# Kernel tuning notes

Hardware: AMD Instinct MI355X
Metric: run time of the kernel (lower is better)

## Reference

```python
import jax, jax.numpy as jnp
import numpy as np

ATOM_FDIM = 133
BOND_FDIM = 147
HIDDEN = 300
DEPTH = 3
N_ATOMS = 100000
N_BONDS = 200000
MAX_NB = 6
N_MOLS = 4000


def setup_inputs() -> dict:
    key = jax.random.key(0)
    ks = jax.random.split(key, 10)
    f_atoms = jax.random.normal(ks[0], (N_ATOMS, ATOM_FDIM), dtype=jnp.float32)
    f_bonds = jax.random.normal(ks[1], (N_BONDS, BOND_FDIM), dtype=jnp.float32)
    a2b = jax.random.randint(ks[2], (N_ATOMS, MAX_NB), 0, N_BONDS)
    b2a = jax.random.randint(ks[3], (N_BONDS,), 0, N_ATOMS)
    b2revb = jax.random.randint(ks[4], (N_BONDS,), 0, N_BONDS)
    atom2mol = jnp.sort(jax.random.randint(ks[5], (N_ATOMS,), 0, N_MOLS))
    s = 1.0 / np.sqrt(HIDDEN)
    W_i = jax.random.uniform(ks[6], (BOND_FDIM, HIDDEN), jnp.float32, -s, s)
    W_h = jax.random.uniform(ks[7], (HIDDEN, HIDDEN), jnp.float32, -s, s)
    W_o_w = jax.random.uniform(ks[8], (ATOM_FDIM + HIDDEN, HIDDEN), jnp.float32, -s, s)
    W_o_b = jax.random.uniform(ks[9], (HIDDEN,), jnp.float32, -s, s)
    return {"f_atoms": f_atoms, "f_bonds": f_bonds, "a2b": a2b, "b2a": b2a,
            "b2revb": b2revb, "atom2mol": atom2mol, "W_i": W_i, "W_h": W_h,
            "W_o_w": W_o_w, "W_o_b": W_o_b}


def reference(f_atoms, f_bonds, a2b, b2a, b2revb, atom2mol, W_i, W_h, W_o_w, W_o_b):
    # input = W_i(f_bonds); message = act(input)
    inp = f_bonds @ W_i                      # [n_bonds, hidden]
    message = jax.nn.relu(inp)
    for _ in range(DEPTH - 1):
        # gather neighbor bond messages per atom and sum: [n_atoms, max_nb, h] -> [n_atoms, h]
        a_message = message[a2b].sum(axis=1)
        rev_message = message[b2revb]        # [n_bonds, hidden]
        message = a_message[b2a] - rev_message
        message = jax.nn.relu(inp + message @ W_h)
    # final atom-level aggregation
    a_message = message[a2b].sum(axis=1)     # [n_atoms, hidden]
    a_input = jnp.concatenate([f_atoms, a_message], axis=1)
    atom_hiddens = jax.nn.relu(a_input @ W_o_w + W_o_b)
    # segment mean pooling over molecules
    sums = jax.ops.segment_sum(atom_hiddens, atom2mol, num_segments=N_MOLS)
    counts = jax.ops.segment_sum(jnp.ones((atom_hiddens.shape[0],), atom_hiddens.dtype),
                                 atom2mol, num_segments=N_MOLS)
    mol_vecs = sums / jnp.maximum(counts, 1.0)[:, None]  # zero vec for empty mols
    return mol_vecs
```

## Files before the change

kernel.cpp:

```cpp
#include <hip/hip_runtime.h>
#include <stdint.h>

#define ATOM_FDIM 133
#define BOND_FDIM 147
#define HIDDEN    300
#define N_ATOMS   100000
#define N_BONDS   200000
#define MAX_NB    6
#define N_MOLS    4000

#define NPAD 320
#define KP_I 160
#define KP_H 320
#define KP_O 448
#define LDA  304
#define CPR  38

typedef unsigned short u16;
typedef short bf16x8 __attribute__((ext_vector_type(8)));
typedef float f32x4 __attribute__((ext_vector_type(4)));

__device__ __forceinline__ u16 f2bu(float f) {
    unsigned u = __float_as_uint(f);
    u += 0x7FFFu + ((u >> 16) & 1u);
    return (u16)(u >> 16);
}
__device__ __forceinline__ float bu2f(u16 b) { return __uint_as_float(((unsigned)b) << 16); }

#define AS1 __attribute__((address_space(1)))
#define AS3 __attribute__((address_space(3)))
__device__ __forceinline__ void gl_lds16(const void* g, void* l) {
    __builtin_amdgcn_global_load_lds((const AS1 void*)g, (AS3 void*)l, 16, 0, 0);
}

template <int EPI>
__global__ __launch_bounds__(256, 3) void mm_k(
    const u16* __restrict__ A, int lda,
    const u16* __restrict__ Wt, int ldw,
    const float* __restrict__ bias,
    u16* __restrict__ out0, int ldo0,
    u16* __restrict__ out1, int ldo1,
    int M, int NT)
{
    __shared__ __align__(16) u16 As[2][64 * 32];
    __shared__ __align__(16) u16 Bs[2][320 * 32];

    const int t    = threadIdx.x;
    const int lane = t & 63, wid = t >> 6;
    const int fl   = lane & 15, fh = lane >> 4;
    const int m0   = blockIdx.x * 64;
    const int wr   = wid >> 1, wc = wid & 1;

    int arow = m0 + wid * 16 + fl;
    if (arow > M - 1) arow = M - 1;
    const unsigned offA = (unsigned)arow * (unsigned)lda * 2u + (unsigned)fh * 16u;
    unsigned offB[5];
    #pragma unroll
    for (int j = 0; j < 5; ++j)
        offB[j] = (unsigned)((wid + 4 * j) * 16 + fl) * (unsigned)ldw * 2u + (unsigned)fh * 16u;

    f32x4 acc[2][10] = {};

    {
        gl_lds16((const char*)A + (size_t)offA, (char*)&As[0][wid * 512]);
        #pragma unroll
        for (int j = 0; j < 5; ++j)
            gl_lds16((const char*)Wt + (size_t)offB[j], (char*)&Bs[0][(wid + 4 * j) * 512]);
    }

    for (int tt = 0; tt < NT; ++tt) {
        const int cur = tt & 1, nxt = cur ^ 1;
        const unsigned kb = (tt + 1 < NT) ? (unsigned)(tt + 1) * 64u : 0u;
        gl_lds16((const char*)A + (size_t)(offA + kb), (char*)&As[nxt][wid * 512]);
        #pragma unroll
        for (int j = 0; j < 5; ++j)
            gl_lds16((const char*)Wt + (size_t)(offB[j] + kb), (char*)&Bs[nxt][(wid + 4 * j) * 512]);

        asm volatile("s_waitcnt vmcnt(6)" ::: "memory");
        __builtin_amdgcn_s_barrier();

        bf16x8 af[2], bfv[10];
        #pragma unroll
        for (int m = 0; m < 2; ++m)
            af[m] = *reinterpret_cast<const bf16x8*>(&As[cur][(wr * 2 + m) * 512 + lane * 8]);
        #pragma unroll
        for (int n = 0; n < 10; ++n)
            bfv[n] = *reinterpret_cast<const bf16x8*>(&Bs[cur][(wc * 10 + n) * 512 + lane * 8]);
        #pragma unroll
        for (int m = 0; m < 2; ++m)
            #pragma unroll
            for (int n = 0; n < 10; ++n)
                acc[m][n] = __builtin_amdgcn_mfma_f32_16x16x32_bf16(af[m], bfv[n], acc[m][n], 0, 0, 0);

        __builtin_amdgcn_s_barrier();
    }

    #pragma unroll
    for (int m = 0; m < 2; ++m) {
        #pragma unroll
        for (int r = 0; r < 4; ++r) {
            const int row = m0 + wr * 32 + m * 16 + fh * 4 + r;
            if (row >= M) continue;
            #pragma unroll
            for (int n = 0; n < 10; ++n) {
                const int col = wc * 160 + n * 16 + fl;
                if (col >= HIDDEN) continue;
                const float v = acc[m][n][r];
                if (EPI == 0) {
                    out0[(size_t)row * ldo0 + col] = f2bu(v);
                    out1[(size_t)row * ldo1 + col] = f2bu(fmaxf(v, 0.f));
                } else if (EPI == 1) {
                    out0[(size_t)row * ldo0 + col] = f2bu(v);
                } else {
                    out0[(size_t)row * ldo0 + col] = f2bu(fmaxf(v + bias[col], 0.f));
                }
            }
        }
    }
}

__global__ __launch_bounds__(256) void wconv_k(const float* __restrict__ W, int Ks, int Kp,
                                               u16* __restrict__ Wt)
{
    const int id = blockIdx.x * 256 + threadIdx.x;
    if (id >= NPAD * Kp) return;
    const int n = id / Kp, k = id - n * Kp;
    const float v = (n < HIDDEN && k < Ks) ? W[(size_t)k * HIDDEN + n] : 0.f;
    Wt[id] = f2bu(v);
}

__global__ __launch_bounds__(256) void fbconv_k(const float* __restrict__ fb, u16* __restrict__ dst)
{
    const int id = blockIdx.x * 256 + threadIdx.x;
    if (id >= N_BONDS * KP_I) return;
    const int r = id / KP_I, k = id - r * KP_I;
    dst[id] = f2bu(k < BOND_FDIM ? fb[(size_t)r * BOND_FDIM + k] : 0.f);
}

__global__ __launch_bounds__(256) void agg_k(const u16* __restrict__ src,
                                             const int* __restrict__ a2b,
                                             u16* __restrict__ dst)
{
    const int c = blockIdx.x * 256 + threadIdx.x;
    if (c >= N_ATOMS * CPR) return;
    const int a = c / CPR, q = c - a * CPR;
    const int h = q * 8;
    const int* nb = a2b + (size_t)a * MAX_NB;
    float s[8] = {};
    #pragma unroll
    for (int j = 0; j < MAX_NB; ++j) {
        const int r = nb[j];
        union { uint4 u; u16 s[8]; } x;
        x.u = *(const uint4*)(src + (size_t)r * LDA + h);
        #pragma unroll
        for (int e = 0; e < 8; ++e) s[e] += bu2f(x.s[e]);
    }
    union { uint4 u; u16 s[8]; } o;
    #pragma unroll
    for (int e = 0; e < 8; ++e) o.s[e] = f2bu(s[e]);
    *(uint4*)(dst + (size_t)a * LDA + h) = o.u;
}

__global__ __launch_bounds__(256) void comb_k(const u16* __restrict__ inp,
                                              const u16* __restrict__ aY,
                                              const u16* __restrict__ Y,
                                              const int* __restrict__ b2a,
                                              const int* __restrict__ b2revb,
                                              u16* __restrict__ msg)
{
    const int c = blockIdx.x * 256 + threadIdx.x;
    if (c >= N_BONDS * CPR) return;
    const int b = c / CPR, q = c - b * CPR;
    const int h = q * 8;
    const int ia = b2a[b], ir = b2revb[b];
    union { uint4 u; u16 s[8]; } xi, xa, xy, o;
    xi.u = *(const uint4*)(inp + (size_t)b * LDA + h);
    xa.u = *(const uint4*)(aY + (size_t)ia * LDA + h);
    xy.u = *(const uint4*)(Y + (size_t)ir * LDA + h);
    #pragma unroll
    for (int j = 0; j < 8; ++j)
        o.s[j] = f2bu(fmaxf(bu2f(xi.s[j]) + bu2f(xa.s[j]) - bu2f(xy.s[j]), 0.f));
    *(uint4*)(msg + (size_t)b * LDA + h) = o.u;
}

__global__ __launch_bounds__(256) void concat_k(const float* __restrict__ fa,
                                                const u16* __restrict__ amsg,
                                                u16* __restrict__ dst)
{
    const int id = blockIdx.x * 256 + threadIdx.x;
    if (id >= N_ATOMS * KP_O) return;
    const int a = id / KP_O, k = id - a * KP_O;
    float v;
    if (k < ATOM_FDIM)                 v = fa[(size_t)a * ATOM_FDIM + k];
    else if (k < ATOM_FDIM + HIDDEN)   v = bu2f(amsg[(size_t)a * LDA + (k - ATOM_FDIM)]);
    else                               v = 0.f;
    dst[id] = f2bu(v);
}

__global__ __launch_bounds__(320) void pool_k(const u16* __restrict__ ah,
                                              const int* __restrict__ a2m,
                                              float* __restrict__ out)
{
    const int m = blockIdx.x;
    int lo, hi;
    { int l = 0, r = N_ATOMS;
      while (l < r) { int mid = (l + r) >> 1; if (a2m[mid] < m) l = mid + 1; else r = mid; }
      lo = l; }
    { int l = lo, r = N_ATOMS;
      while (l < r) { int mid = (l + r) >> 1; if (a2m[mid] < m + 1) l = mid + 1; else r = mid; }
      hi = l; }
    const float inv = 1.0f / (float)((hi - lo) > 1 ? (hi - lo) : 1);
    const int h = threadIdx.x;
    if (h >= HIDDEN) return;
    float s = 0.f;
    for (int a = lo; a < hi; ++a) s += bu2f(ah[(size_t)a * LDA + h]);
    out[(size_t)m * HIDDEN + h] = s * inv;
}

extern "C" void kernel_launch(void* const* d_in, const int* in_sizes, int n_in,
                              void* d_out, int out_size, void* d_ws, size_t ws_size,
                              hipStream_t stream)
{
    const float* f_atoms  = (const float*)d_in[0];
    const float* f_bonds  = (const float*)d_in[1];
    const int*   a2b      = (const int*)d_in[2];
    const int*   b2a      = (const int*)d_in[3];
    const int*   b2revb   = (const int*)d_in[4];
    const int*   atom2mol = (const int*)d_in[5];
    const float* W_i      = (const float*)d_in[6];
    const float* W_h      = (const float*)d_in[7];
    const float* W_o_w    = (const float*)d_in[8];
    const float* W_o_b    = (const float*)d_in[9];
    float* out = (float*)d_out;

    char* p = (char*)d_ws;
    auto alloc = [&](size_t bytes) { char* r = p; p += (bytes + 255) & ~(size_t)255; return r; };
    u16* inp = (u16*)alloc(((size_t)N_BONDS + 16) * LDA * 2);
    u16* msg = (u16*)alloc(((size_t)N_BONDS + 16) * LDA * 2);
    u16* Yb  = (u16*)alloc(((size_t)N_BONDS + 16) * LDA * 2);
    u16* aY  = (u16*)alloc(((size_t)N_ATOMS + 16) * LDA * 2);
    u16* Wti = (u16*)alloc((size_t)NPAD * KP_I * 2);
    u16* Wth = (u16*)alloc((size_t)NPAD * KP_H * 2);
    u16* Wto = (u16*)alloc((size_t)NPAD * KP_O * 2 + 4096);
    if ((size_t)(p - (char*)d_ws) > ws_size) return;

    u16* fb16   = Yb;
    u16* concat = Yb;
    u16* ah     = msg;

    const dim3 blk(256);
    auto g1 = [](long long n) { return dim3((unsigned)((n + 255) / 256)); };
    const dim3 gB((N_BONDS + 63) / 64);
    const dim3 gA((N_ATOMS + 63) / 64);

    wconv_k<<<g1((long long)NPAD * KP_I), blk, 0, stream>>>(W_i, BOND_FDIM, KP_I, Wti);
    wconv_k<<<g1((long long)NPAD * KP_H), blk, 0, stream>>>(W_h, HIDDEN, KP_H, Wth);
    wconv_k<<<g1((long long)NPAD * KP_O), blk, 0, stream>>>(W_o_w, ATOM_FDIM + HIDDEN, KP_O, Wto);
    fbconv_k<<<g1((long long)N_BONDS * KP_I), blk, 0, stream>>>(f_bonds, fb16);

    mm_k<0><<<gB, blk, 0, stream>>>(fb16, KP_I, Wti, KP_I, nullptr,
                                    inp, LDA, msg, LDA, N_BONDS, KP_I / 32);

    for (int it = 0; it < 2; ++it) {
        mm_k<1><<<gB, blk, 0, stream>>>(msg, LDA, Wth, KP_H, nullptr,
                                        Yb, LDA, nullptr, 0, N_BONDS, KP_H / 32);
        agg_k<<<g1((long long)N_ATOMS * CPR), blk, 0, stream>>>(Yb, a2b, aY);
        comb_k<<<g1((long long)N_BONDS * CPR), blk, 0, stream>>>(inp, aY, Yb, b2a, b2revb, msg);
    }

    agg_k<<<g1((long long)N_ATOMS * CPR), blk, 0, stream>>>(msg, a2b, aY);
    concat_k<<<g1((long long)N_ATOMS * KP_O), blk, 0, stream>>>(f_atoms, aY, concat);
    mm_k<2><<<gA, blk, 0, stream>>>(concat, KP_O, Wto, KP_O, W_o_b,
                                    ah, LDA, nullptr, 0, N_ATOMS, KP_O / 32);
    pool_k<<<dim3(N_MOLS), dim3(320), 0, stream>>>(ah, atom2mol, out);
}
```

Measured before the change: 1.000 ms.

## Rework GEMM kernel: 128-row tiles, 512 threads, triple-buffered LDS, prepacked weights

The bf16 MFMA GEMM moves from 64-row tiles with 256 threads to 128-row tiles with 512 threads (8 waves) and a 384-wide padded N. LDS goes from double to triple buffering with a prefetch distance of two K-steps. Each K-step is split into two MFMA phases with setprio, interleaved with loads of the next tiles. Weights are prepacked into the exact MFMA fragment layout so B loads become contiguous. The aim is better latency hiding and more reuse of each weight load, at the cost of more padded N columns, more LDS, and lower occupancy per CU.

```diff
diff --git a/kernel.cpp b/kernel.cpp
--- a/kernel.cpp
+++ b/kernel.cpp
@@ -9,13 +9,17 @@
 #define MAX_NB    6
 #define N_MOLS    4000
 
-#define NPAD 320
 #define KP_I 160
 #define KP_H 320
 #define KP_O 448
 #define LDA  304
 #define CPR  38
 
+#define TM   128
+#define NPAD 384
+#define ACH  8
+#define BCH  24
+
 typedef unsigned short u16;
 typedef short bf16x8 __attribute__((ext_vector_type(8)));
 typedef float f32x4 __attribute__((ext_vector_type(4)));
@@ -34,65 +38,94 @@
 }
 
 template <int EPI>
-__global__ __launch_bounds__(256, 3) void mm_k(
+__global__ __launch_bounds__(512, 2) void mm_k(
     const u16* __restrict__ A, int lda,
-    const u16* __restrict__ Wt, int ldw,
+    const u16* __restrict__ Wp,
     const float* __restrict__ bias,
     u16* __restrict__ out0, int ldo0,
     u16* __restrict__ out1, int ldo1,
     int M, int NT)
 {
-    __shared__ __align__(16) u16 As[2][64 * 32];
-    __shared__ __align__(16) u16 Bs[2][320 * 32];
+    __shared__ __align__(16) u16 As[3][ACH * 512];
+    __shared__ __align__(16) u16 Bs[3][BCH * 512];
 
     const int t    = threadIdx.x;
     const int lane = t & 63, wid = t >> 6;
     const int fl   = lane & 15, fh = lane >> 4;
-    const int m0   = blockIdx.x * 64;
+    const int m0   = blockIdx.x * TM;
     const int wr   = wid >> 1, wc = wid & 1;
 
     int arow = m0 + wid * 16 + fl;
     if (arow > M - 1) arow = M - 1;
-    const unsigned offA = (unsigned)arow * (unsigned)lda * 2u + (unsigned)fh * 16u;
-    unsigned offB[5];
-    #pragma unroll
-    for (int j = 0; j < 5; ++j)
-        offB[j] = (unsigned)((wid + 4 * j) * 16 + fl) * (unsigned)ldw * 2u + (unsigned)fh * 16u;
-
-    f32x4 acc[2][10] = {};
+    const size_t srcA = (size_t)arow * (size_t)lda * 2u + (size_t)(fh * 16);
+    const size_t srcB = (size_t)(3 * wid) * 1024u + (size_t)lane * 16u;
+
+    char* ldsA_of[3] = { (char*)As[0] + wid * 1024, (char*)As[1] + wid * 1024,
+                         (char*)As[2] + wid * 1024 };
+    char* ldsB_of[3] = { (char*)Bs[0] + 3 * wid * 1024, (char*)Bs[1] + 3 * wid * 1024,
+                         (char*)Bs[2] + 3 * wid * 1024 };
+
+    f32x4 acc[2][12] = {};
 
     {
-        gl_lds16((const char*)A + (size_t)offA, (char*)&As[0][wid * 512]);
-        #pragma unroll
-        for (int j = 0; j < 5; ++j)
-            gl_lds16((const char*)Wt + (size_t)offB[j], (char*)&Bs[0][(wid + 4 * j) * 512]);
-    }
-
+        gl_lds16((const char*)A + srcA, ldsA_of[0]);
+        #pragma unroll
+        for (int j = 0; j < 3; ++j)
+            gl_lds16((const char*)Wp + srcB + (size_t)j * 1024, ldsB_of[0] + j * 1024);
+        gl_lds16((const char*)A + srcA + 64, ldsA_of[1]);
+        #pragma unroll
+        for (int j = 0; j < 3; ++j)
+            gl_lds16((const char*)Wp + (size_t)BCH * 1024 + srcB + (size_t)j * 1024,
+                     ldsB_of[1] + j * 1024);
+    }
+    asm volatile("s_waitcnt vmcnt(4)" ::: "memory");
+    __builtin_amdgcn_s_barrier();
+
+    int cur = 0;
     for (int tt = 0; tt < NT; ++tt) {
-        const int cur = tt & 1, nxt = cur ^ 1;
-        const unsigned kb = (tt + 1 < NT) ? (unsigned)(tt + 1) * 64u : 0u;
-        gl_lds16((const char*)A + (size_t)(offA + kb), (char*)&As[nxt][wid * 512]);
-        #pragma unroll
-        for (int j = 0; j < 5; ++j)
-            gl_lds16((const char*)Wt + (size_t)(offB[j] + kb), (char*)&Bs[nxt][(wid + 4 * j) * 512]);
-
-        asm volatile("s_waitcnt vmcnt(6)" ::: "memory");
+        const int nx2 = (cur >= 1) ? cur - 1 : 2;
+        int w2 = tt + 2; if (w2 >= NT) w2 -= NT;
+        const u16* as_c = As[cur];
+        const u16* bs_c = Bs[cur];
+        const size_t kbA = (size_t)w2 * 64u;
+        const size_t kbB = (size_t)w2 * (BCH * 1024u);
+
+        bf16x8 af0, af1, bfv[12];
+
+        af0 = *reinterpret_cast<const bf16x8*>(&as_c[(wr * 2 + 0) * 512 + lane * 8]);
+        af1 = *reinterpret_cast<const bf16x8*>(&as_c[(wr * 2 + 1) * 512 + lane * 8]);
+        #pragma unroll
+        for (int n = 0; n < 6; ++n)
+            bfv[n] = *reinterpret_cast<const bf16x8*>(&bs_c[(wc * 12 + n) * 512 + lane * 8]);
+        gl_lds16((const char*)A + srcA + kbA, ldsA_of[nx2]);
+        gl_lds16((const char*)Wp + kbB + srcB, ldsB_of[nx2]);
         __builtin_amdgcn_s_barrier();
-
-        bf16x8 af[2], bfv[10];
-        #pragma unroll
-        for (int m = 0; m < 2; ++m)
-            af[m] = *reinterpret_cast<const bf16x8*>(&As[cur][(wr * 2 + m) * 512 + lane * 8]);
-        #pragma unroll
-        for (int n = 0; n < 10; ++n)
-            bfv[n] = *reinterpret_cast<const bf16x8*>(&Bs[cur][(wc * 10 + n) * 512 + lane * 8]);
-        #pragma unroll
-        for (int m = 0; m < 2; ++m)
-            #pragma unroll
-            for (int n = 0; n < 10; ++n)
-                acc[m][n] = __builtin_amdgcn_mfma_f32_16x16x32_bf16(af[m], bfv[n], acc[m][n], 0, 0, 0);
-
+        __builtin_amdgcn_s_setprio(1);
+        #pragma unroll
+        for (int n = 0; n < 6; ++n) {
+            acc[0][n] = __builtin_amdgcn_mfma_f32_16x16x32_bf16(af0, bfv[n], acc[0][n], 0, 0, 0);
+            acc[1][n] = __builtin_amdgcn_mfma_f32_16x16x32_bf16(af1, bfv[n], acc[1][n], 0, 0, 0);
+        }
+        __builtin_amdgcn_s_setprio(0);
         __builtin_amdgcn_s_barrier();
+
+        #pragma unroll
+        for (int n = 6; n < 12; ++n)
+            bfv[n] = *reinterpret_cast<const bf16x8*>(&bs_c[(wc * 12 + n) * 512 + lane * 8]);
+        gl_lds16((const char*)Wp + kbB + srcB + 1024, ldsB_of[nx2] + 1024);
+        gl_lds16((const char*)Wp + kbB + srcB + 2048, ldsB_of[nx2] + 2048);
+        asm volatile("s_waitcnt vmcnt(4)" ::: "memory");
+        __builtin_amdgcn_s_barrier();
+        __builtin_amdgcn_s_setprio(1);
+        #pragma unroll
+        for (int n = 6; n < 12; ++n) {
+            acc[0][n] = __builtin_amdgcn_mfma_f32_16x16x32_bf16(af0, bfv[n], acc[0][n], 0, 0, 0);
+            acc[1][n] = __builtin_amdgcn_mfma_f32_16x16x32_bf16(af1, bfv[n], acc[1][n], 0, 0, 0);
+        }
+        __builtin_amdgcn_s_setprio(0);
+        __builtin_amdgcn_s_barrier();
+
+        cur = (cur == 2) ? 0 : cur + 1;
     }
 
     #pragma unroll
@@ -102,8 +135,8 @@
             const int row = m0 + wr * 32 + m * 16 + fh * 4 + r;
             if (row >= M) continue;
             #pragma unroll
-            for (int n = 0; n < 10; ++n) {
-                const int col = wc * 160 + n * 16 + fl;
+            for (int n = 0; n < 12; ++n) {
+                const int col = wc * 192 + n * 16 + fl;
                 if (col >= HIDDEN) continue;
                 const float v = acc[m][n][r];
                 if (EPI == 0) {
@@ -119,14 +152,18 @@
     }
 }
 
-__global__ __launch_bounds__(256) void wconv_k(const float* __restrict__ W, int Ks, int Kp,
-                                               u16* __restrict__ Wt)
+__global__ __launch_bounds__(256) void wconv_k(const float* __restrict__ W, int Ks, int NT,
+                                               u16* __restrict__ Wp)
 {
     const int id = blockIdx.x * 256 + threadIdx.x;
-    if (id >= NPAD * Kp) return;
-    const int n = id / Kp, k = id - n * Kp;
-    const float v = (n < HIDDEN && k < Ks) ? W[(size_t)k * HIDDEN + n] : 0.f;
-    Wt[id] = f2bu(v);
+    if (id >= NT * BCH * 512) return;
+    const int block = id >> 9, rem = id & 511;
+    const int l = rem >> 3, e = rem & 7;
+    const int c = block % BCH, kt = block / BCH;
+    const int col = c * 16 + (l & 15);
+    const int k   = kt * 32 + (l >> 4) * 8 + e;
+    const float v = (col < HIDDEN && k < Ks) ? W[(size_t)k * HIDDEN + col] : 0.f;
+    Wp[id] = f2bu(v);
 }
 
 __global__ __launch_bounds__(256) void fbconv_k(const float* __restrict__ fb, u16* __restrict__ dst)
@@ -239,9 +276,9 @@
     u16* msg = (u16*)alloc(((size_t)N_BONDS + 16) * LDA * 2);
     u16* Yb  = (u16*)alloc(((size_t)N_BONDS + 16) * LDA * 2);
     u16* aY  = (u16*)alloc(((size_t)N_ATOMS + 16) * LDA * 2);
-    u16* Wti = (u16*)alloc((size_t)NPAD * KP_I * 2);
-    u16* Wth = (u16*)alloc((size_t)NPAD * KP_H * 2);
-    u16* Wto = (u16*)alloc((size_t)NPAD * KP_O * 2 + 4096);
+    u16* Wpi = (u16*)alloc((size_t)(KP_I / 32) * BCH * 512 * 2);
+    u16* Wph = (u16*)alloc((size_t)(KP_H / 32) * BCH * 512 * 2);
+    u16* Wpo = (u16*)alloc((size_t)(KP_O / 32) * BCH * 512 * 2);
     if ((size_t)(p - (char*)d_ws) > ws_size) return;
 
     u16* fb16   = Yb;
@@ -250,27 +287,28 @@
 
     const dim3 blk(256);
     auto g1 = [](long long n) { return dim3((unsigned)((n + 255) / 256)); };
-    const dim3 gB((N_BONDS + 63) / 64);
-    const dim3 gA((N_ATOMS + 63) / 64);
-
-    wconv_k<<<g1((long long)NPAD * KP_I), blk, 0, stream>>>(W_i, BOND_FDIM, KP_I, Wti);
-    wconv_k<<<g1((long long)NPAD * KP_H), blk, 0, stream>>>(W_h, HIDDEN, KP_H, Wth);
-    wconv_k<<<g1((long long)NPAD * KP_O), blk, 0, stream>>>(W_o_w, ATOM_FDIM + HIDDEN, KP_O, Wto);
+    const dim3 blk5(512);
+    const dim3 gB((N_BONDS + TM - 1) / TM);
+    const dim3 gA((N_ATOMS + TM - 1) / TM);
+
+    wconv_k<<<g1((long long)(KP_I / 32) * BCH * 512), blk, 0, stream>>>(W_i, BOND_FDIM, KP_I / 32, Wpi);
+    wconv_k<<<g1((long long)(KP_H / 32) * BCH * 512), blk, 0, stream>>>(W_h, HIDDEN, KP_H / 32, Wph);
+    wconv_k<<<g1((long long)(KP_O / 32) * BCH * 512), blk, 0, stream>>>(W_o_w, ATOM_FDIM + HIDDEN, KP_O / 32, Wpo);
     fbconv_k<<<g1((long long)N_BONDS * KP_I), blk, 0, stream>>>(f_bonds, fb16);
 
-    mm_k<0><<<gB, blk, 0, stream>>>(fb16, KP_I, Wti, KP_I, nullptr,
-                                    inp, LDA, msg, LDA, N_BONDS, KP_I / 32);
+    mm_k<0><<<gB, blk5, 0, stream>>>(fb16, KP_I, Wpi, nullptr,
+                                     inp, LDA, msg, LDA, N_BONDS, KP_I / 32);
 
     for (int it = 0; it < 2; ++it) {
-        mm_k<1><<<gB, blk, 0, stream>>>(msg, LDA, Wth, KP_H, nullptr,
-                                        Yb, LDA, nullptr, 0, N_BONDS, KP_H / 32);
+        mm_k<1><<<gB, blk5, 0, stream>>>(msg, LDA, Wph, nullptr,
+                                         Yb, LDA, nullptr, 0, N_BONDS, KP_H / 32);
         agg_k<<<g1((long long)N_ATOMS * CPR), blk, 0, stream>>>(Yb, a2b, aY);
         comb_k<<<g1((long long)N_BONDS * CPR), blk, 0, stream>>>(inp, aY, Yb, b2a, b2revb, msg);
     }
 
     agg_k<<<g1((long long)N_ATOMS * CPR), blk, 0, stream>>>(msg, a2b, aY);
     concat_k<<<g1((long long)N_ATOMS * KP_O), blk, 0, stream>>>(f_atoms, aY, concat);
-    mm_k<2><<<gA, blk, 0, stream>>>(concat, KP_O, Wto, KP_O, W_o_b,
-                                    ah, LDA, nullptr, 0, N_ATOMS, KP_O / 32);
+    mm_k<2><<<gA, blk5, 0, stream>>>(concat, KP_O, Wpo, W_o_b,
+                                     ah, LDA, nullptr, 0, N_ATOMS, KP_O / 32);
     pool_k<<<dim3(N_MOLS), dim3(320), 0, stream>>>(ah, atom2mol, out);
 }
```

Measured after the change: 945.4 us. 1.06x faster.
